# Performance work log

Measured on AMD Instinct MI355X. Metric: run time of the kernel, lower is better.

Reference implementation:

```python
import jax, jax.numpy as jnp
import numpy as np

B, T, C = 2, 2048, 1024
N = 16
D = C // N  # 64


def setup_inputs() -> dict:
    key = jax.random.key(0)
    ks = jax.random.split(key, 5)
    s = 1.0 / np.sqrt(C)  # lecun_normal-ish scale for Dense kernels
    return {
        "src": jax.random.normal(ks[0], (B, T, C), jnp.float32),
        "mask": jnp.ones((B, T), jnp.float32),  # unused on causal path
        "Wq": jax.random.normal(ks[1], (C, C), jnp.float32) * s,
        "bq": jnp.zeros((C,), jnp.float32),
        "Wk": jax.random.normal(ks[2], (C, C), jnp.float32) * s,
        "bk": jnp.zeros((C,), jnp.float32),
        "Wv": jax.random.normal(ks[3], (C, C), jnp.float32) * s,
        "bv": jnp.zeros((C,), jnp.float32),
        "Wo": jax.random.normal(ks[4], (C, C), jnp.float32) * s,
        "bo": jnp.zeros((C,), jnp.float32),
    }


def reference(src, mask, Wq, bq, Wk, bk, Wv, bv, Wo, bo):
    # QKV projections -> [B, N, T, D]
    def heads(x):
        return x.reshape(B, T, N, D).transpose(0, 2, 1, 3)

    q = heads(src @ Wq + bq)
    k = heads(src @ Wk + bk)
    v = heads(src @ Wv + bv)

    # scores [B, N, T, T], causal mask, softmax
    scores = jnp.einsum("bntd,bnsd->bnts", q, k) / jnp.sqrt(jnp.float32(D))
    causal = jnp.tril(jnp.ones((T, T), bool))
    scores = jnp.where(causal, scores, -jnp.inf)
    attn = jax.nn.softmax(scores, axis=-1)

    # weighted values, merge heads, output projection (dropout deterministic)
    out = jnp.einsum("bnts,bnsd->bntd", attn, v)
    out = out.transpose(0, 2, 1, 3).reshape(B, T, C)
    return out @ Wo + bo
```

## Files before the change

kernel.cpp:

```cpp
#include <hip/hip_runtime.h>

typedef __bf16 bf16;
typedef bf16 bf16x8 __attribute__((ext_vector_type(8)));
typedef float f32x4 __attribute__((ext_vector_type(4)));
typedef unsigned short u16;
typedef u16 u16x4 __attribute__((ext_vector_type(4)));
typedef u16 u16x8 __attribute__((ext_vector_type(8)));

typedef const __attribute__((address_space(1))) void* gptr_t;
typedef __attribute__((address_space(3))) void* sptr_t;

__device__ __forceinline__ void async16(const void* g, void* l) {
  __builtin_amdgcn_global_load_lds((gptr_t)g, (sptr_t)l, 16, 0, 0);
}
__device__ __forceinline__ u16 f2bf(float v) {
  return __builtin_bit_cast(u16, (bf16)v);
}

__device__ __forceinline__ size_t paddr(int r, int k, int KT) {
  return (size_t)((r >> 4) * KT + (k >> 5)) * 512 + ((k >> 3) & 3) * 128 +
         (r & 15) * 8 + (k & 7);
}

__global__ void kPrep(const float* __restrict__ src, u16* __restrict__ Xp,
                      const float* __restrict__ Wq, const float* __restrict__ Wk,
                      const float* __restrict__ Wv, const float* __restrict__ Wo,
                      u16* __restrict__ Wp) {
  __shared__ float tile[32][33];
  const int bid = blockIdx.x, tid = threadIdx.x;
  if (bid < 4096) {
    const int i = (bid * 256 + tid) * 4;
    const int m = i >> 10, k = i & 1023;
    float4 v = *(const float4*)&src[i];
    u16x4 o = {f2bf(v.x), f2bf(v.y), f2bf(v.z), f2bf(v.w)};
    *(u16x4*)&Xp[paddr(m, k, 32)] = o;
  } else {
    const int t = bid - 4096;
    const int z = t >> 10, tt = t & 1023;
    const float* W = (z == 0) ? Wq : (z == 1) ? Wk : (z == 2) ? Wv : Wo;
    const int n0 = (tt & 31) * 32, k0 = (tt >> 5) * 32;
    const int tx = tid & 31, ty = tid >> 5;
#pragma unroll
    for (int j = 0; j < 4; ++j)
      tile[ty + j * 8][tx] = W[(size_t)(k0 + ty + j * 8) * 1024 + n0 + tx];
    __syncthreads();
    if (tid < 128) {
      const int sub = tid >> 6, l = tid & 63, hi = l >> 4, lo = l & 15;
      u16x8 o;
#pragma unroll
      for (int e = 0; e < 8; ++e) o[e] = f2bf(tile[hi * 8 + e][sub * 16 + lo]);
      const size_t ad = (size_t)z * 1048576 +
                        (size_t)(((n0 >> 4) + sub) * 32 + (k0 >> 5)) * 512 +
                        hi * 128 + lo * 8;
      *(u16x8*)&Wp[ad] = o;
    }
  }
}

__global__ __launch_bounds__(256, 3) void kGemmQKV(
    const u16* __restrict__ A, const u16* __restrict__ Bt,
    const float* __restrict__ b0, const float* __restrict__ b1,
    const float* __restrict__ b2, u16* __restrict__ outQ) {
  __shared__ __align__(16) u16 Als[2][8 * 512];
  const int tid = threadIdx.x, l = tid & 63, w = tid >> 6;
  const int bid = (blockIdx.x & 7) * 96 + (blockIdx.x >> 3);
  const int mb = bid & 31, nb = bid >> 5;
  const int mbase = mb * 128, nbase = nb * 128;
  const int wr = (w >> 1) * 64, wc = (w & 1) * 64;
  const int hi = l >> 4, lo = l & 15;

  const u16* bb[4];
#pragma unroll
  for (int nf = 0; nf < 4; ++nf)
    bb[nf] = &Bt[(size_t)((nbase + wc + nf * 16) >> 4) * 16384 + l * 8];

  f32x4 acc[4][4];
#pragma unroll
  for (int i = 0; i < 4; ++i)
#pragma unroll
    for (int j = 0; j < 4; ++j) acc[i][j] = (f32x4){0.f, 0.f, 0.f, 0.f};

  auto stageA = [&](int bufi, int kt) {
#pragma unroll
    for (int i = 0; i < 2; ++i) {
      const int fr = w * 2 + i;
      async16(&A[(size_t)((mb * 8 + fr) * 32 + kt) * 512 + l * 8],
              &Als[bufi][fr * 512]);
    }
  };

  bf16x8 breg[2][4];
  stageA(0, 0);
#pragma unroll
  for (int nf = 0; nf < 4; ++nf) breg[0][nf] = *(const bf16x8*)&bb[nf][0];

  auto step = [&](int kt, bf16x8 (&bc)[4], bf16x8 (&bn)[4]) {
    const int cur = kt & 1;
    if (kt < 31) {
      stageA(cur ^ 1, kt + 1);
#pragma unroll
      for (int nf = 0; nf < 4; ++nf)
        bn[nf] = *(const bf16x8*)&bb[nf][(kt + 1) * 512];
      asm volatile("s_waitcnt vmcnt(6)" ::: "memory");
    } else {
      asm volatile("s_waitcnt vmcnt(0)" ::: "memory");
    }
    __builtin_amdgcn_s_barrier();
    __builtin_amdgcn_sched_barrier(0);

    bf16x8 a[4];
#pragma unroll
    for (int mf = 0; mf < 4; ++mf)
      a[mf] = *(const bf16x8*)&Als[cur][((w >> 1) * 4 + mf) * 512 + l * 8];
#pragma unroll
    for (int mf = 0; mf < 4; ++mf)
#pragma unroll
      for (int nf = 0; nf < 4; ++nf)
        acc[mf][nf] = __builtin_amdgcn_mfma_f32_16x16x32_bf16(a[mf], bc[nf],
                                                              acc[mf][nf], 0, 0, 0);
    __builtin_amdgcn_s_barrier();
  };

  for (int kt2 = 0; kt2 < 32; kt2 += 2) {
    step(kt2, breg[0], breg[1]);
    step(kt2 + 1, breg[1], breg[0]);
  }

  u16* Qo = outQ;
  u16* Ko = outQ + 4 * 1048576;
  u16* Vo = outQ + 8 * 1048576;
  const int mat = nb >> 3;
  const float* bias = (mat == 0) ? b0 : (mat == 1) ? b1 : b2;
  const float qs = (mat == 0) ? 0.1803368801f : 1.0f;
#pragma unroll
  for (int nf = 0; nf < 4; ++nf) {
    const int n = nbase + wc + nf * 16 + lo;
    const int cc = n & 1023, h = cc >> 6, d = cc & 63;
    const float bsv = bias[cc];
#pragma unroll
    for (int mf = 0; mf < 4; ++mf)
#pragma unroll
      for (int r = 0; r < 4; ++r) {
        const int m = mbase + wr + mf * 16 + hi * 4 + r;
        const int bb_ = m >> 11, t = m & 2047;
        const u16 hv = f2bf((acc[mf][nf][r] + bsv) * qs);
        const size_t hd = (size_t)(bb_ * 16 + h) * 131072;
        if (mat < 2) {
          (mat == 0 ? Qo : Ko)[hd + paddr(t, d, 2)] = hv;
        } else {
          Vo[hd + paddr(d, t, 64)] = hv;
        }
      }
  }
}

__global__ __launch_bounds__(256, 2) void kGemmO(
    const u16* __restrict__ A, const u16* __restrict__ Bt,
    const float* __restrict__ b0, float* __restrict__ outF) {
  __shared__ __align__(16) u16 Als[2][8 * 512];
  const int tid = threadIdx.x, l = tid & 63, w = tid >> 6;
  const int bid = (blockIdx.x & 7) * 64 + (blockIdx.x >> 3);
  const int mb = bid & 31, nb = bid >> 5;
  const int mbase = mb * 128, nbase = nb * 64;
  const int wr = (w >> 1) * 64, wc = (w & 1) * 32;
  const int hi = l >> 4, lo = l & 15;

  const u16* bb[2];
#pragma unroll
  for (int nf = 0; nf < 2; ++nf)
    bb[nf] = &Bt[(size_t)((nbase + wc + nf * 16) >> 4) * 16384 + l * 8];

  f32x4 acc[4][2];
#pragma unroll
  for (int i = 0; i < 4; ++i)
#pragma unroll
    for (int j = 0; j < 2; ++j) acc[i][j] = (f32x4){0.f, 0.f, 0.f, 0.f};

  auto stageA = [&](int bufi, int kt) {
#pragma unroll
    for (int i = 0; i < 2; ++i) {
      const int fr = w * 2 + i;
      async16(&A[(size_t)((mb * 8 + fr) * 32 + kt) * 512 + l * 8],
              &Als[bufi][fr * 512]);
    }
  };

  bf16x8 breg[2][2];
  stageA(0, 0);
#pragma unroll
  for (int nf = 0; nf < 2; ++nf) breg[0][nf] = *(const bf16x8*)&bb[nf][0];

  auto step = [&](int kt, bf16x8 (&bc)[2], bf16x8 (&bn)[2]) {
    const int cur = kt & 1;
    if (kt < 31) {
      stageA(cur ^ 1, kt + 1);
#pragma unroll
      for (int nf = 0; nf < 2; ++nf)
        bn[nf] = *(const bf16x8*)&bb[nf][(kt + 1) * 512];
      asm volatile("s_waitcnt vmcnt(4)" ::: "memory");
    } else {
      asm volatile("s_waitcnt vmcnt(0)" ::: "memory");
    }
    __builtin_amdgcn_s_barrier();
    __builtin_amdgcn_sched_barrier(0);

    bf16x8 a[4];
#pragma unroll
    for (int mf = 0; mf < 4; ++mf)
      a[mf] = *(const bf16x8*)&Als[cur][((w >> 1) * 4 + mf) * 512 + l * 8];
#pragma unroll
    for (int mf = 0; mf < 4; ++mf)
#pragma unroll
      for (int nf = 0; nf < 2; ++nf)
        acc[mf][nf] = __builtin_amdgcn_mfma_f32_16x16x32_bf16(a[mf], bc[nf],
                                                              acc[mf][nf], 0, 0, 0);
    __builtin_amdgcn_s_barrier();
  };

  for (int kt2 = 0; kt2 < 32; kt2 += 2) {
    step(kt2, breg[0], breg[1]);
    step(kt2 + 1, breg[1], breg[0]);
  }

#pragma unroll
  for (int nf = 0; nf < 2; ++nf) {
    const int n = nbase + wc + nf * 16 + lo;
    const float bsv = b0[n];
#pragma unroll
    for (int mf = 0; mf < 4; ++mf)
#pragma unroll
      for (int r = 0; r < 4; ++r) {
        const int m = mbase + wr + mf * 16 + hi * 4 + r;
        outF[(size_t)m * 1024 + n] = acc[mf][nf][r] + bsv;
      }
  }
}

#define PSTR 36
__global__ __launch_bounds__(512, 2) void kAttn(const u16* __restrict__ Qp,
                                                const u16* __restrict__ Kp,
                                                const u16* __restrict__ Vp,
                                                u16* __restrict__ AOp) {
  __shared__ __align__(16) u16 Pl[8][16 * PSTR];
  __shared__ __align__(16) float Red[4][2][16][64];
  __shared__ float RedL[4][2][64];
  const int tid = threadIdx.x, l = tid & 63, w = tid >> 6;
  const int grp = w >> 1, half = w & 1;
  const int g = l >> 4, c = l & 15;
  const int id = blockIdx.x;
  const int xcd = id & 7, rem = id >> 3;
  const int pi = rem & 7, bh = (rem >> 3) * 8 + xcd;
  const int qt0 = 31 - pi, qt1 = 16 + pi, qt2 = 15 - pi, qt3 = pi;
  const size_t head = (size_t)bh * 131072;
  const u16* Kh = Kp + head;
  const u16* Vh = Vp + head;

  bf16x8 aq0[2], aq1[2], aq2[2], aq3[2];
#pragma unroll
  for (int ks = 0; ks < 2; ++ks) {
    aq0[ks] = *(const bf16x8*)&Qp[head + (size_t)((qt0 * 4 + grp) * 2 + ks) * 512 + l * 8];
    aq1[ks] = *(const bf16x8*)&Qp[head + (size_t)((qt1 * 4 + grp) * 2 + ks) * 512 + l * 8];
    aq2[ks] = *(const bf16x8*)&Qp[head + (size_t)((qt2 * 4 + grp) * 2 + ks) * 512 + l * 8];
    aq3[ks] = *(const bf16x8*)&Qp[head + (size_t)((qt3 * 4 + grp) * 2 + ks) * 512 + l * 8];
  }

  f32x4 acc0[4], acc1[4], acc2[4], acc3[4];
#pragma unroll
  for (int i = 0; i < 4; ++i) {
    acc0[i] = (f32x4){0.f, 0.f, 0.f, 0.f};
    acc1[i] = (f32x4){0.f, 0.f, 0.f, 0.f};
    acc2[i] = (f32x4){0.f, 0.f, 0.f, 0.f};
    acc3[i] = (f32x4){0.f, 0.f, 0.f, 0.f};
  }
  float l0 = 0.f, l1 = 0.f, l2 = 0.f, l3 = 0.f;

  bf16x8 kr[4];
#pragma unroll
  for (int f = 0; f < 4; ++f)
    kr[f] = *(const bf16x8*)&Kh[(size_t)((half * 2 + (f >> 1)) * 2 + (f & 1)) * 512 + l * 8];
  bf16x8 vr[4];

  auto qkTile = [&](const bf16x8* aq, f32x4* sT) {
#pragma unroll
    for (int sf = 0; sf < 2; ++sf)
#pragma unroll
      for (int ks = 0; ks < 2; ++ks)
        sT[sf] = __builtin_amdgcn_mfma_f32_16x16x32_bf16(kr[sf * 2 + ks], aq[ks],
                                                         sT[sf], 0, 0, 0);
  };

  auto finishTile = [&](const f32x4* sT, bool diag, f32x4* accO, float& lpart) {
    float v[8];
#pragma unroll
    for (int sf = 0; sf < 2; ++sf)
#pragma unroll
      for (int r = 0; r < 4; ++r) v[sf * 4 + r] = sT[sf][r];
    if (diag) {
      const int qin = grp * 16 + c;
#pragma unroll
      for (int sf = 0; sf < 2; ++sf)
#pragma unroll
        for (int r = 0; r < 4; ++r)
          if (half * 32 + sf * 16 + g * 4 + r > qin) v[sf * 4 + r] = -__builtin_inff();
    }
    float p[8];
#pragma unroll
    for (int i = 0; i < 8; ++i) p[i] = __builtin_exp2f(v[i]);
#pragma unroll
    for (int sf = 0; sf < 2; ++sf) {
      u16x4 q4 = {f2bf(p[sf * 4 + 0]), f2bf(p[sf * 4 + 1]),
                  f2bf(p[sf * 4 + 2]), f2bf(p[sf * 4 + 3])};
      *(u16x4*)&Pl[w][c * PSTR + sf * 16 + g * 4] = q4;
    }
    lpart += ((p[0] + p[1]) + (p[2] + p[3])) + ((p[4] + p[5]) + (p[6] + p[7]));
    bf16x8 pf = *(const bf16x8*)&Pl[w][c * PSTR + g * 8];
#pragma unroll
    for (int nd = 0; nd < 4; ++nd)
      accO[nd] = __builtin_amdgcn_mfma_f32_16x16x32_bf16(pf, vr[nd], accO[nd], 0, 0, 0);
  };

  const int nst = qt0 + 1;
  for (int st = 0; st < nst; ++st) {
#pragma unroll
    for (int nd = 0; nd < 4; ++nd)
      vr[nd] = *(const bf16x8*)&Vh[(size_t)(nd * 64 + st * 2 + half) * 512 + l * 8];

    f32x4 sT[2];
    if (st <= qt3) {
#pragma unroll
      for (int i = 0; i < 2; ++i) sT[i] = (f32x4){0.f, 0.f, 0.f, 0.f};
      qkTile(aq3, sT);
      finishTile(sT, st == qt3, acc3, l3);
    }
    if (st <= qt2) {
#pragma unroll
      for (int i = 0; i < 2; ++i) sT[i] = (f32x4){0.f, 0.f, 0.f, 0.f};
      qkTile(aq2, sT);
      finishTile(sT, st == qt2, acc2, l2);
    }
    if (st <= qt1) {
#pragma unroll
      for (int i = 0; i < 2; ++i) sT[i] = (f32x4){0.f, 0.f, 0.f, 0.f};
      qkTile(aq1, sT);
      finishTile(sT, st == qt1, acc1, l1);
    }
    {
#pragma unroll
      for (int i = 0; i < 2; ++i) sT[i] = (f32x4){0.f, 0.f, 0.f, 0.f};
      qkTile(aq0, sT);
      if (st < qt0) {
#pragma unroll
        for (int f = 0; f < 4; ++f)
          kr[f] = *(const bf16x8*)&Kh[(size_t)(((st + 1) * 4 + half * 2 + (f >> 1)) * 2 +
                                               (f & 1)) * 512 + l * 8];
      }
      finishTile(sT, st == qt0, acc0, l0);
    }
  }

  const int b = bh >> 4, h = bh & 15;
  auto writeOut = [&](int qt, const f32x4* accO, float lc) {
#pragma unroll
    for (int r = 0; r < 4; ++r) {
      const float lr = __shfl(lc, g * 4 + r);
      const float rin = 1.0f / lr;
      const int mg = b * 2048 + qt * 64 + grp * 16 + g * 4 + r;
#pragma unroll
      for (int nd = 0; nd < 4; ++nd) {
        const int col = h * 64 + nd * 16 + c;
        AOp[paddr(mg, col, 32)] = f2bf(accO[nd][r] * rin);
      }
    }
  };
  auto combinePair = [&](f32x4* accX, float lX, int qtX, f32x4* accY, float lY,
                         int qtY) {
    float lcX = lX + __shfl_xor(lX, 16);
    lcX += __shfl_xor(lcX, 32);
    float lcY = lY + __shfl_xor(lY, 16);
    lcY += __shfl_xor(lcY, 32);
    __syncthreads();
    if (half) {
#pragma unroll
      for (int nd = 0; nd < 4; ++nd)
#pragma unroll
        for (int r = 0; r < 4; ++r) {
          Red[grp][0][nd * 4 + r][l] = accX[nd][r];
          Red[grp][1][nd * 4 + r][l] = accY[nd][r];
        }
      RedL[grp][0][l] = lcX;
      RedL[grp][1][l] = lcY;
    }
    __syncthreads();
    if (!half) {
#pragma unroll
      for (int nd = 0; nd < 4; ++nd)
#pragma unroll
        for (int r = 0; r < 4; ++r) {
          accX[nd][r] += Red[grp][0][nd * 4 + r][l];
          accY[nd][r] += Red[grp][1][nd * 4 + r][l];
        }
      writeOut(qtX, accX, lcX + RedL[grp][0][l]);
      writeOut(qtY, accY, lcY + RedL[grp][1][l]);
    }
  };
  combinePair(acc0, l0, qt0, acc1, l1, qt1);
  combinePair(acc2, l2, qt2, acc3, l3, qt3);
}

extern "C" void kernel_launch(void* const* d_in, const int* in_sizes, int n_in,
                              void* d_out, int out_size, void* d_ws, size_t ws_size,
                              hipStream_t stream) {
  const float* src = (const float*)d_in[0];
  const float* Wq = (const float*)d_in[2];
  const float* bq = (const float*)d_in[3];
  const float* Wk = (const float*)d_in[4];
  const float* bk = (const float*)d_in[5];
  const float* Wv = (const float*)d_in[6];
  const float* bv = (const float*)d_in[7];
  const float* Wo = (const float*)d_in[8];
  const float* bo = (const float*)d_in[9];
  float* out = (float*)d_out;

  char* ws = (char*)d_ws;
  u16* Wp = (u16*)(ws);
  u16* Xp = (u16*)(ws + 8ull * 1024 * 1024);
  u16* Qb = (u16*)(ws + 16ull * 1024 * 1024);
  u16* AOp = (u16*)(ws + 40ull * 1024 * 1024);

  kPrep<<<dim3(8192), dim3(256), 0, stream>>>(src, Xp, Wq, Wk, Wv, Wo, Wp);
  kGemmQKV<<<dim3(768), dim3(256), 0, stream>>>(Xp, Wp, bq, bk, bv, Qb);
  kAttn<<<dim3(256), dim3(512), 0, stream>>>(Qb, Qb + 4 * 1048576,
                                             Qb + 8 * 1048576, AOp);
  kGemmO<<<dim3(512), dim3(256), 0, stream>>>(AOp, Wp + 3ull * 1048576, bo, out);
}
```

Baseline: 104.3 us.

## Stage K/V tiles into double-buffered LDS with async global-to-LDS loads

Replaces the per-wave direct global loads of K and V fragments with a cooperative double-buffered LDS staging scheme. Each wave issues global_load_lds for one K and one V chunk of the next tile while the current tile is computed, then reads fragments from LDS. Two waves that share a half used to load the same K/V data redundantly, and this removes that duplicate global traffic. The cost is a block-wide barrier plus a vmcnt(0) wait every iteration and 32KB of extra LDS, which could hurt occupancy at 2 blocks per CU.

```diff
diff --git a/kernel.cpp b/kernel.cpp
--- a/kernel.cpp
+++ b/kernel.cpp
@@ -241,6 +241,8 @@
                                                 const u16* __restrict__ Kp,
                                                 const u16* __restrict__ Vp,
                                                 u16* __restrict__ AOp) {
+  __shared__ __align__(16) u16 Ksh[2][8 * 512];
+  __shared__ __align__(16) u16 Vsh[2][8 * 512];
   __shared__ __align__(16) u16 Pl[8][16 * PSTR];
   __shared__ __align__(16) float Red[4][2][16][64];
   __shared__ float RedL[4][2][64];
@@ -274,11 +276,13 @@
   }
   float l0 = 0.f, l1 = 0.f, l2 = 0.f, l3 = 0.f;
 
-  bf16x8 kr[4];
-#pragma unroll
-  for (int f = 0; f < 4; ++f)
-    kr[f] = *(const bf16x8*)&Kh[(size_t)((half * 2 + (f >> 1)) * 2 + (f & 1)) * 512 + l * 8];
-  bf16x8 vr[4];
+  auto stageKV = [&](int buf, int st) {
+    async16(&Kh[(size_t)(st * 8 + w) * 512 + l * 8], &Ksh[buf][w * 512]);
+    async16(&Vh[(size_t)((w >> 1) * 64 + st * 2 + (w & 1)) * 512 + l * 8],
+            &Vsh[buf][w * 512]);
+  };
+
+  bf16x8 kr[4], vr[4];
 
   auto qkTile = [&](const bf16x8* aq, f32x4* sT) {
 #pragma unroll
@@ -319,11 +323,24 @@
       accO[nd] = __builtin_amdgcn_mfma_f32_16x16x32_bf16(pf, vr[nd], accO[nd], 0, 0, 0);
   };
 
+  stageKV(0, 0);
+  asm volatile("s_waitcnt vmcnt(0)" ::: "memory");
+  __builtin_amdgcn_s_barrier();
+
   const int nst = qt0 + 1;
   for (int st = 0; st < nst; ++st) {
+    const int cur = st & 1;
+    if (st + 1 < nst) stageKV(cur ^ 1, st + 1);
+
+#pragma unroll
+    for (int sf = 0; sf < 2; ++sf)
+#pragma unroll
+      for (int ks = 0; ks < 2; ++ks)
+        kr[sf * 2 + ks] =
+            *(const bf16x8*)&Ksh[cur][(half * 4 + sf * 2 + ks) * 512 + l * 8];
 #pragma unroll
     for (int nd = 0; nd < 4; ++nd)
-      vr[nd] = *(const bf16x8*)&Vh[(size_t)(nd * 64 + st * 2 + half) * 512 + l * 8];
+      vr[nd] = *(const bf16x8*)&Vsh[cur][(nd * 2 + half) * 512 + l * 8];
 
     f32x4 sT[2];
     if (st <= qt3) {
@@ -348,14 +365,12 @@
 #pragma unroll
       for (int i = 0; i < 2; ++i) sT[i] = (f32x4){0.f, 0.f, 0.f, 0.f};
       qkTile(aq0, sT);
-      if (st < qt0) {
-#pragma unroll
-        for (int f = 0; f < 4; ++f)
-          kr[f] = *(const bf16x8*)&Kh[(size_t)(((st + 1) * 4 + half * 2 + (f >> 1)) * 2 +
-                                               (f & 1)) * 512 + l * 8];
-      }
       finishTile(sT, st == qt0, acc0, l0);
     }
+
+    asm volatile("s_waitcnt vmcnt(0)" ::: "memory");
+    __builtin_amdgcn_s_barrier();
+    __builtin_amdgcn_sched_barrier(0);
   }
 
   const int b = bh >> 4, h = bh & 15;
```

Result: slower. 115.1 us (+10.4%).
